# Kernel optimization log

Hardware: AMD Instinct MI355X
Metric: run time of the kernel (lower is better)

The kernel has to match this reference:

```python
import jax
import jax.numpy as jnp
import numpy as np

B, R, C, Q, D = 16, 2048, 81, 65, 1024
K = 1024          # pre-NMS candidate cap (fixed-shape stand-in for torch's dynamic filtering)
DET = 100         # detections_per_img
IMG = 640.0       # square image size (clip bound)
SCORE_THRESH = 0.05
NMS_THRESH = 0.5
MIN_SIZE = 0.01
BBOX_CLIP = float(np.log(1000.0 / 16.0))  # torchvision BoxCoder bbox_xform_clip
WX, WY, WW, WH = 10.0, 10.0, 5.0, 5.0     # BoxCoder weights


def setup_inputs() -> dict:
    key = jax.random.key(0)
    k1, k2, k3, k4, k5, k6 = jax.random.split(key, 6)
    class_logits = 2.0 * jax.random.normal(k1, (B, R, C), jnp.float32)
    quantity_logits = jax.random.normal(k2, (B, R, Q), jnp.float32)
    box_features = jax.random.normal(k3, (B, R, D), jnp.float32)
    box_regression = 0.5 * jax.random.normal(k4, (B, R, C * 4), jnp.float32)
    cxcy = jax.random.uniform(k5, (B, R, 2), jnp.float32, 0.0, IMG)
    wh = jax.random.uniform(k6, (B, R, 2), jnp.float32, 10.0, 80.0)
    x1y1 = jnp.clip(cxcy - 0.5 * wh, 0.0, IMG)
    x2y2 = jnp.clip(cxcy + 0.5 * wh, 0.0, IMG)
    proposals = jnp.concatenate([x1y1, x2y2], axis=-1)
    return {
        'class_logits': class_logits,
        'quantity_logits': quantity_logits,
        'box_features': box_features,
        'box_regression': box_regression,
        'proposals': proposals,
    }


def _decode(deltas, props):
    # deltas: [R, C, 4], props: [R, 4] -> boxes [R, C, 4] (torchvision BoxCoder.decode)
    pw = props[:, 2] - props[:, 0]
    ph = props[:, 3] - props[:, 1]
    pcx = props[:, 0] + 0.5 * pw
    pcy = props[:, 1] + 0.5 * ph
    dx = deltas[..., 0] / WX
    dy = deltas[..., 1] / WY
    dw = jnp.minimum(deltas[..., 2] / WW, BBOX_CLIP)
    dh = jnp.minimum(deltas[..., 3] / WH, BBOX_CLIP)
    cx = dx * pw[:, None] + pcx[:, None]
    cy = dy * ph[:, None] + pcy[:, None]
    w = jnp.exp(dw) * pw[:, None]
    h = jnp.exp(dh) * ph[:, None]
    return jnp.stack([cx - 0.5 * w, cy - 0.5 * h, cx + 0.5 * w, cy + 0.5 * h], axis=-1)


def _iou_matrix(b):
    # b: [K, 4] -> pairwise IoU [K, K]
    area = (b[:, 2] - b[:, 0]) * (b[:, 3] - b[:, 1])
    lt = jnp.maximum(b[:, None, :2], b[None, :, :2])
    rb = jnp.minimum(b[:, None, 2:], b[None, :, 2:])
    whv = jnp.clip(rb - lt, 0.0)
    inter = whv[..., 0] * whv[..., 1]
    return inter / (area[:, None] + area[None, :] - inter + 1e-9)


def _process_image(logits, qlogits, feats, reg, props):
    # decode + clip
    boxes = jnp.clip(_decode(reg.reshape(R, C, 4), props), 0.0, IMG)  # [R, C, 4]
    scores = jax.nn.softmax(logits, axis=-1)                          # [R, C]
    quant = jnp.argmax(qlogits, axis=-1).astype(jnp.int32)            # [R]
    # drop background class 0, flatten to M = R*(C-1)
    fb = boxes[:, 1:, :].reshape(-1, 4)
    fs = scores[:, 1:].reshape(-1)
    fl = jnp.broadcast_to(jnp.arange(1, C, dtype=jnp.int32), (R, C - 1)).reshape(-1)
    fi = jnp.broadcast_to(jnp.arange(R, dtype=jnp.int32)[:, None], (R, C - 1)).reshape(-1)
    bw = fb[:, 2] - fb[:, 0]
    bh = fb[:, 3] - fb[:, 1]
    valid = (fs > SCORE_THRESH) & (bw >= MIN_SIZE) & (bh >= MIN_SIZE)
    # top-K candidates by masked score (sorted desc)
    top_s, top_i = jax.lax.top_k(jnp.where(valid, fs, -1.0), K)
    cb = fb[top_i]          # [K, 4]
    cl = fl[top_i]          # [K]
    ci = fi[top_i]          # [K] row index into proposals/features
    cv = top_s > 0.0        # candidate validity (score_thresh > 0)
    # batched NMS via per-class coordinate offset
    ob = cb + (cl.astype(jnp.float32) * (IMG + 1.0))[:, None]
    iou = _iou_matrix(ob)
    ar = jnp.arange(K)

    def body(i, keep):
        sup = (iou[i] > NMS_THRESH) & (ar > i)
        return jnp.where(keep[i] & cv[i], keep & ~sup, keep)

    keep = jax.lax.fori_loop(0, K, body, cv) & cv
    # first DET survivors in score order
    det_s, det_i = jax.lax.top_k(jnp.where(keep, top_s, -1.0), DET)
    dv = det_s > 0.0
    m = dv.astype(jnp.float32)
    db = cb[det_i] * m[:, None]
    dl = jnp.where(dv, cl[det_i], 0)
    di = ci[det_i]
    dq = jnp.where(dv, quant[di], 0)
    df = feats[di] * m[:, None]   # irregular gather of box features by surviving row idx
    ds = jnp.where(dv, det_s, 0.0)
    return db, ds, dl, dq, df, dv


def reference(class_logits, quantity_logits, box_features, box_regression, proposals):
    # returns (boxes [B,DET,4], scores [B,DET], labels [B,DET] i32,
    #          quantities [B,DET] i32, features [B,DET,D], valid [B,DET] bool)
    return jax.vmap(_process_image)(class_logits, quantity_logits, box_features,
                                    box_regression, proposals)
```

## Files before the change

### kernel.cpp

```cpp
#include <hip/hip_runtime.h>
#include <math.h>

#define NB 16
#define NR 2048
#define NC 81
#define NQ 65
#define ND 1024
#define NK 1024
#define NDET 100
#define NBLK 512
#define BSLOT 64
#define HBINS 5184
#define CH 256
#define L2CAP 384
#define LRCAP 1536
#define BBC 4.135166556742356f

#define O_BOX   0
#define O_SCORE (NB*NDET*4)
#define O_LABEL (O_SCORE + NB*NDET)
#define O_QUANT (O_LABEL + NB*NDET)
#define O_FEAT  (O_QUANT + NB*NDET)
#define O_VALID (O_FEAT + (size_t)NB*NDET*ND)

#define WS_CAND  ((size_t)0)
#define WS_GHIST (WS_CAND + (size_t)NB*NBLK*BSLOT*8)
#define WS_DETCB (WS_GHIST + (size_t)NB*HBINS*4)
#define WS_DETM  (WS_DETCB + (size_t)NB*NDET*16)
#define WS_DETS  (WS_DETM + (size_t)NB*NDET*4)
#define WS_CNT   (WS_DETS + (size_t)NB*NDET*4)

__device__ __forceinline__ float4 decode_box(float4 d, float pw, float ph,
                                             float pcx, float pcy) {
    float dx = d.x / 10.0f, dy = d.y / 10.0f;
    float dw = fminf(d.z / 5.0f, BBC), dh = fminf(d.w / 5.0f, BBC);
    float cx = dx * pw + pcx, cy = dy * ph + pcy;
    float w = expf(dw) * pw, h = expf(dh) * ph;
    float4 r;
    r.x = fminf(fmaxf(cx - 0.5f * w, 0.0f), 640.0f);
    r.y = fminf(fmaxf(cy - 0.5f * h, 0.0f), 640.0f);
    r.z = fminf(fmaxf(cx + 0.5f * w, 0.0f), 640.0f);
    r.w = fminf(fmaxf(cy + 0.5f * h, 0.0f), 640.0f);
    return r;
}

__global__ __launch_bounds__(256) void k_stage1(
    const float* __restrict__ logits, const float* __restrict__ reg,
    const float* __restrict__ props, unsigned long long* __restrict__ cand,
    int* __restrict__ cnt, unsigned int* __restrict__ ghist) {
    __shared__ unsigned long long sl[BSLOT];
    __shared__ int scnt;
    int b = blockIdx.x >> 9;
    int blk = blockIdx.x & (NBLK - 1);
    int wid = threadIdx.x >> 6;
    int lane = threadIdx.x & 63;
    int r = blk * 4 + wid;
    int row = b * NR + r;
    if (threadIdx.x == 0) scnt = 0;
    __syncthreads();

    const float* Lrow = logits + (size_t)row * NC;
    float v0 = Lrow[lane];
    float v1 = (lane < NC - 64) ? Lrow[64 + lane] : -1e30f;
    float mx = fmaxf(v0, v1);
    #pragma unroll
    for (int o = 32; o; o >>= 1) mx = fmaxf(mx, __shfl_xor(mx, o));
    float e = expf(v0 - mx) + ((lane < NC - 64) ? expf(v1 - mx) : 0.0f);
    float sm = e;
    #pragma unroll
    for (int o = 32; o; o >>= 1) sm += __shfl_xor(sm, o);
    float thr_lo = mx + logf(0.05f * sm) - 0.01f;

    const float* P = props + (size_t)row * 4;
    float p0 = P[0], p1 = P[1], p2 = P[2], p3 = P[3];
    float pw = p2 - p0, ph = p3 - p1;
    float pcx = p0 + 0.5f * pw, pcy = p1 + 0.5f * ph;
    const float* G = reg + (size_t)row * (NC * 4);

    #pragma unroll
    for (int pass = 0; pass < 2; ++pass) {
        int cc = lane + pass * 64;
        if (cc < NC - 1) {
            int c = cc + 1;
            float lc = Lrow[c];
            if (lc > thr_lo) {
                float p = expf(lc - mx) / sm;
                float4 d = *(const float4*)(G + 4 * c);
                float4 bx = decode_box(d, pw, ph, pcx, pcy);
                float bw = bx.z - bx.x, bh = bx.w - bx.y;
                if (p > 0.05f && bw >= 0.01f && bh >= 0.01f) {
                    int m = r * 80 + cc;
                    int pos = atomicAdd(&scnt, 1);
                    if (pos < BSLOT) {
                        sl[pos] = ((unsigned long long)__float_as_uint(p) << 32) |
                                  (unsigned)(~(unsigned)m);
                        unsigned bin = (__float_as_uint(p) - 0x3D000000u) >> 13;
                        atomicAdd(&ghist[b * HBINS + bin], 1u);
                    }
                }
            }
        }
    }
    __syncthreads();
    int n = scnt < BSLOT ? scnt : BSLOT;
    unsigned long long* dst = cand + ((size_t)b * NBLK + blk) * BSLOT;
    for (int i = threadIdx.x; i < n; i += 256) dst[i] = sl[i];
    if (threadIdx.x == 0) cnt[b * NBLK + blk] = n;
}

__global__ __launch_bounds__(1024) void k_fused(
    const unsigned long long* __restrict__ cand, const int* __restrict__ cnt,
    const unsigned int* __restrict__ ghist,
    const float* __restrict__ reg, const float* __restrict__ props,
    int* __restrict__ det_m, float* __restrict__ det_s,
    float4* __restrict__ det_cb) {
    __shared__ union {
        unsigned int hist[HBINS];
        unsigned long long sortedRest[LRCAP];
    } u;
    __shared__ unsigned long long list2[L2CAP], sorted2[L2CAP];
    __shared__ unsigned long long listRest[LRCAP];
    __shared__ float4 boff[L2CAP], bclip[L2CAP];
    __shared__ int scn[NBLK];
    __shared__ int s_c2, s_cR, s_b1, s_b2, s_A, s_need;
    int b = blockIdx.x, tid = threadIdx.x;
    const unsigned long long* cnd = cand + (size_t)b * NBLK * BSLOT;

    for (int i = tid; i < HBINS; i += 1024) u.hist[i] = ghist[b * HBINS + i];
    if (tid < NBLK) scn[tid] = cnt[b * NBLK + tid];
    if (tid == 0) { s_c2 = 0; s_cR = 0; s_b1 = 0; s_b2 = 0; s_A = 0; s_need = 0; }
    __syncthreads();

    if (tid < 64) {
        int lane = tid, base = lane * 81;
        unsigned partial = 0;
        for (int j = 0; j < 81; ++j) partial += u.hist[base + j];
        unsigned incl = partial;
        #pragma unroll
        for (int o = 1; o < 64; o <<= 1) {
            unsigned t = __shfl_up(incl, o);
            if (lane >= o) incl += t;
        }
        unsigned total = __shfl(incl, 63);
        unsigned suffix = total - incl;
        if (suffix < NK && suffix + partial >= NK) {
            unsigned A = suffix;
            for (int bb = base + 80; bb >= base; --bb) {
                unsigned An = A + u.hist[bb];
                if (An >= NK) { s_b1 = bb; break; }
                A = An;
            }
        }
        if (suffix < CH && suffix + partial >= CH) {
            unsigned A = suffix;
            for (int bb = base + 80; bb >= base; --bb) {
                unsigned An = A + u.hist[bb];
                if (An >= CH) { s_b2 = bb; break; }
                A = An;
            }
        }
    }
    __syncthreads();
    int b1 = s_b1, b2 = s_b2;

    for (int i = tid; i < NBLK * BSLOT; i += 1024) {
        if ((i & (BSLOT - 1)) < scn[i >> 6]) {
            unsigned long long key = cnd[i];
            int bin = (int)(((unsigned)(key >> 32) - 0x3D000000u) >> 13);
            if (bin >= b2) {
                int p = atomicAdd(&s_c2, 1);
                if (p < L2CAP) list2[p] = key;
            } else if (bin >= b1) {
                int p = atomicAdd(&s_cR, 1);
                if (p < LRCAP) listRest[p] = key;
            }
        }
    }
    __syncthreads();
    int T2 = s_c2 < L2CAP ? s_c2 : L2CAP;
    int TR = s_cR < LRCAP ? s_cR : LRCAP;
    int S = T2 + TR;
    int cap = S < NK ? S : NK;
    int limit1 = T2 < cap ? T2 : cap;

    if (tid < T2) {
        unsigned long long k0 = list2[tid];
        int rk = 0;
        for (int j = 0; j < T2; ++j) rk += (list2[j] > k0);
        sorted2[rk] = k0;
    }
    __syncthreads();

    if (tid < limit1) {
        unsigned long long key = sorted2[tid];
        int m = (int)(~(unsigned)key);
        int r = m / 80, c = m - r * 80 + 1;
        size_t row = (size_t)b * NR + r;
        float4 P = *(const float4*)(props + row * 4);
        float pw = P.z - P.x, ph = P.w - P.y;
        float pcx = P.x + 0.5f * pw, pcy = P.y + 0.5f * ph;
        float4 d = *(const float4*)(reg + row * (NC * 4) + 4 * c);
        float4 bx = decode_box(d, pw, ph, pcx, pcy);
        bclip[tid] = bx;
        float off = (float)c * 641.0f;
        float4 o = {bx.x + off, bx.y + off, bx.z + off, bx.w + off};
        boff[tid] = o;
    }
    __syncthreads();

    int lane = tid & 63;
    float4 a0 = {0, 0, 0, 0}, a1 = {0, 0, 0, 0};
    int A = 0;
    if (tid < 64) {
        unsigned long long nk_ = (limit1 > 0) ? sorted2[0] : 0ull;
        float4 nb_ = (limit1 > 0) ? boff[0] : a0;
        for (int t = 0; t < limit1; ++t) {
            unsigned long long keyt = nk_;
            float4 bt = nb_;
            if (t + 1 < limit1) { nk_ = sorted2[t + 1]; nb_ = boff[t + 1]; }
            float areaB = (bt.z - bt.x) * (bt.w - bt.y);
            float areaA0 = (a0.z - a0.x) * (a0.w - a0.y);
            float ltx = fmaxf(a0.x, bt.x), lty = fmaxf(a0.y, bt.y);
            float rbx = fminf(a0.z, bt.z), rby = fminf(a0.w, bt.w);
            float in0 = fmaxf(rbx - ltx, 0.0f) * fmaxf(rby - lty, 0.0f);
            bool sup = (lane < A) && (in0 / (areaA0 + areaB - in0 + 1e-9f) > 0.5f);
            if (A > 64) {
                float areaA1 = (a1.z - a1.x) * (a1.w - a1.y);
                float l1 = fmaxf(a1.x, bt.x), t1 = fmaxf(a1.y, bt.y);
                float r1 = fminf(a1.z, bt.z), b1f = fminf(a1.w, bt.w);
                float in1 = fmaxf(r1 - l1, 0.0f) * fmaxf(b1f - t1, 0.0f);
                sup |= (lane + 64 < A) &&
                       (in1 / (areaA1 + areaB - in1 + 1e-9f) > 0.5f);
            }
            if (!__any((int)sup)) {
                if (lane == (A & 63)) { if (A < 64) a0 = bt; else a1 = bt; }
                if (lane == 0) {
                    det_m[b * NDET + A] = (int)(~(unsigned)keyt);
                    det_s[b * NDET + A] = __uint_as_float((unsigned)(keyt >> 32));
                    det_cb[b * NDET + A] = bclip[t];
                }
                ++A;
                if (A == NDET) break;
            }
        }
        if (tid == 0) { s_A = A; s_need = (A < NDET && limit1 < cap) ? 1 : 0; }
    }
    __syncthreads();

    if (s_need) {
        for (int t0 = tid; t0 < TR; t0 += 1024) {
            unsigned long long k0 = listRest[t0];
            int rk = 0;
            for (int j = 0; j < TR; ++j) rk += (listRest[j] > k0);
            u.sortedRest[rk] = k0;
        }
        __syncthreads();
        if (tid < 64) {
            int nrest = cap - limit1;
            for (int t = 0; t < nrest && A < NDET; ++t) {
                unsigned long long keyt = u.sortedRest[t];
                int m = (int)(~(unsigned)keyt);
                int r = m / 80, c = m - r * 80 + 1;
                size_t row = (size_t)b * NR + r;
                float4 P = *(const float4*)(props + row * 4);
                float pw = P.z - P.x, ph = P.w - P.y;
                float pcx = P.x + 0.5f * pw, pcy = P.y + 0.5f * ph;
                float4 d = *(const float4*)(reg + row * (NC * 4) + 4 * c);
                float4 bx = decode_box(d, pw, ph, pcx, pcy);
                float off = (float)c * 641.0f;
                float4 bt = {bx.x + off, bx.y + off, bx.z + off, bx.w + off};
                float areaB = (bt.z - bt.x) * (bt.w - bt.y);
                float areaA0 = (a0.z - a0.x) * (a0.w - a0.y);
                float ltx = fmaxf(a0.x, bt.x), lty = fmaxf(a0.y, bt.y);
                float rbx = fminf(a0.z, bt.z), rby = fminf(a0.w, bt.w);
                float in0 = fmaxf(rbx - ltx, 0.0f) * fmaxf(rby - lty, 0.0f);
                bool sup = (lane < A) &&
                           (in0 / (areaA0 + areaB - in0 + 1e-9f) > 0.5f);
                if (A > 64) {
                    float areaA1 = (a1.z - a1.x) * (a1.w - a1.y);
                    float l1 = fmaxf(a1.x, bt.x), t1 = fmaxf(a1.y, bt.y);
                    float r1 = fminf(a1.z, bt.z), b1f = fminf(a1.w, bt.w);
                    float in1 = fmaxf(r1 - l1, 0.0f) * fmaxf(b1f - t1, 0.0f);
                    sup |= (lane + 64 < A) &&
                           (in1 / (areaA1 + areaB - in1 + 1e-9f) > 0.5f);
                }
                if (!__any((int)sup)) {
                    if (lane == (A & 63)) { if (A < 64) a0 = bt; else a1 = bt; }
                    if (lane == 0) {
                        det_m[b * NDET + A] = m;
                        det_s[b * NDET + A] =
                            __uint_as_float((unsigned)(keyt >> 32));
                        det_cb[b * NDET + A] = bx;
                    }
                    ++A;
                }
            }
            if (tid == 0) s_A = A;
        }
        __syncthreads();
    }
    for (int d = s_A + tid; d < NDET; d += 1024) det_m[b * NDET + d] = -1;
}

__global__ __launch_bounds__(256) void k_final(
    const float* __restrict__ feats, const float* __restrict__ qlog,
    const int* __restrict__ det_m, const float* __restrict__ det_s,
    const float4* __restrict__ det_cb, float* __restrict__ out) {
    int bd = blockIdx.x;
    int b = bd / NDET;
    int t = threadIdx.x;
    int m = det_m[bd];
    float4* of = (float4*)(out + O_FEAT + (size_t)bd * ND);
    if (m >= 0) {
        int r = m / 80, c = m - r * 80 + 1;
        size_t row = (size_t)b * NR + r;
        if (t == 0) {
            ((float4*)(out + O_BOX))[bd] = det_cb[bd];
            out[O_SCORE + bd] = det_s[bd];
            out[O_LABEL + bd] = (float)c;
            out[O_VALID + bd] = 1.0f;
        }
        if (t < 64) {
            const float* Qrow = qlog + row * NQ;
            float qv = Qrow[t];
            int qi = t;
            if (t == 0) {
                float q64 = Qrow[64];
                if (q64 > qv) { qv = q64; qi = 64; }
            }
            #pragma unroll
            for (int o = 32; o; o >>= 1) {
                float ov = __shfl_xor(qv, o);
                int oi = __shfl_xor(qi, o);
                if (ov > qv || (ov == qv && oi < qi)) { qv = ov; qi = oi; }
            }
            if (t == 0) out[O_QUANT + bd] = (float)qi;
        }
        const float4* f = (const float4*)(feats + row * ND);
        of[t] = f[t];
    } else {
        if (t == 0) {
            float4 z = {0, 0, 0, 0};
            ((float4*)(out + O_BOX))[bd] = z;
            out[O_SCORE + bd] = 0.0f;
            out[O_LABEL + bd] = 0.0f;
            out[O_QUANT + bd] = 0.0f;
            out[O_VALID + bd] = 0.0f;
        }
        float4 z = {0, 0, 0, 0};
        of[t] = z;
    }
}

extern "C" void kernel_launch(void* const* d_in, const int* in_sizes, int n_in,
                              void* d_out, int out_size, void* d_ws, size_t ws_size,
                              hipStream_t stream) {
    const float* logits = (const float*)d_in[0];
    const float* qlog   = (const float*)d_in[1];
    const float* feats  = (const float*)d_in[2];
    const float* reg    = (const float*)d_in[3];
    const float* props  = (const float*)d_in[4];
    float* out = (float*)d_out;
    char* ws = (char*)d_ws;

    unsigned long long* cand = (unsigned long long*)(ws + WS_CAND);
    unsigned int* ghist = (unsigned int*)(ws + WS_GHIST);
    float4* det_cb = (float4*)(ws + WS_DETCB);
    int* det_m = (int*)(ws + WS_DETM);
    float* det_s = (float*)(ws + WS_DETS);
    int* cnt = (int*)(ws + WS_CNT);

    hipMemsetAsync(ghist, 0, (size_t)NB * HBINS * 4, stream);
    k_stage1<<<NB * NBLK, 256, 0, stream>>>(logits, reg, props, cand, cnt, ghist);
    k_fused<<<NB, 1024, 0, stream>>>(cand, cnt, ghist, reg, props, det_m, det_s,
                                     det_cb);
    k_final<<<NB * NDET, 256, 0, stream>>>(feats, qlog, det_m, det_s, det_cb, out);
}
```

Measured before the change: 294.8 us.

## Fuse final gather into NMS kernel, reuse softmax exps, prefetch features

After: 300.2 us. About the same (+1.8%).

```diff
diff --git a/kernel.cpp b/kernel.cpp
--- a/kernel.cpp
+++ b/kernel.cpp
@@ -25,10 +25,7 @@
 
 #define WS_CAND  ((size_t)0)
 #define WS_GHIST (WS_CAND + (size_t)NB*NBLK*BSLOT*8)
-#define WS_DETCB (WS_GHIST + (size_t)NB*HBINS*4)
-#define WS_DETM  (WS_DETCB + (size_t)NB*NDET*16)
-#define WS_DETS  (WS_DETM + (size_t)NB*NDET*4)
-#define WS_CNT   (WS_DETS + (size_t)NB*NDET*4)
+#define WS_CNT   (WS_GHIST + (size_t)NB*HBINS*4)
 
 __device__ __forceinline__ float4 decode_box(float4 d, float pw, float ph,
                                              float pcx, float pcy) {
@@ -65,11 +62,16 @@
     float mx = fmaxf(v0, v1);
     #pragma unroll
     for (int o = 32; o; o >>= 1) mx = fmaxf(mx, __shfl_xor(mx, o));
-    float e = expf(v0 - mx) + ((lane < NC - 64) ? expf(v1 - mx) : 0.0f);
-    float sm = e;
+    float t0 = expf(v0 - mx);
+    float t1 = (lane < NC - 64) ? expf(v1 - mx) : 0.0f;
+    float sm = t0 + t1;
     #pragma unroll
     for (int o = 32; o; o >>= 1) sm += __shfl_xor(sm, o);
-    float thr_lo = mx + logf(0.05f * sm) - 0.01f;
+
+    float nx0 = __shfl_down(t0, 1);
+    float b64 = __shfl(t1, 0);
+    float tc0 = (lane == 63) ? b64 : nx0;
+    float tc1 = __shfl_down(t1, 1);
 
     const float* P = props + (size_t)row * 4;
     float p0 = P[0], p1 = P[1], p2 = P[2], p3 = P[3];
@@ -80,15 +82,15 @@
     #pragma unroll
     for (int pass = 0; pass < 2; ++pass) {
         int cc = lane + pass * 64;
+        float tc = pass ? tc1 : tc0;
         if (cc < NC - 1) {
-            int c = cc + 1;
-            float lc = Lrow[c];
-            if (lc > thr_lo) {
-                float p = expf(lc - mx) / sm;
+            float p = tc / sm;
+            if (p > 0.05f) {
+                int c = cc + 1;
                 float4 d = *(const float4*)(G + 4 * c);
                 float4 bx = decode_box(d, pw, ph, pcx, pcy);
                 float bw = bx.z - bx.x, bh = bx.w - bx.y;
-                if (p > 0.05f && bw >= 0.01f && bh >= 0.01f) {
+                if (bw >= 0.01f && bh >= 0.01f) {
                     int m = r * 80 + cc;
                     int pos = atomicAdd(&scnt, 1);
                     if (pos < BSLOT) {
@@ -112,8 +114,8 @@
     const unsigned long long* __restrict__ cand, const int* __restrict__ cnt,
     const unsigned int* __restrict__ ghist,
     const float* __restrict__ reg, const float* __restrict__ props,
-    int* __restrict__ det_m, float* __restrict__ det_s,
-    float4* __restrict__ det_cb) {
+    const float* __restrict__ feats, const float* __restrict__ qlog,
+    float* __restrict__ out) {
     __shared__ union {
         unsigned int hist[HBINS];
         unsigned long long sortedRest[LRCAP];
@@ -122,8 +124,12 @@
     __shared__ unsigned long long listRest[LRCAP];
     __shared__ float4 boff[L2CAP], bclip[L2CAP];
     __shared__ int scn[NBLK];
+    __shared__ int acc_m[NDET];
+    __shared__ float acc_s[NDET];
+    __shared__ float4 acc_b[NDET];
     __shared__ int s_c2, s_cR, s_b1, s_b2, s_A, s_need;
     int b = blockIdx.x, tid = threadIdx.x;
+    int lane = tid & 63;
     const unsigned long long* cnd = cand + (size_t)b * NBLK * BSLOT;
 
     for (int i = tid; i < HBINS; i += 1024) u.hist[i] = ghist[b * HBINS + i];
@@ -132,7 +138,7 @@
     __syncthreads();
 
     if (tid < 64) {
-        int lane = tid, base = lane * 81;
+        int base = tid * 81;
         unsigned partial = 0;
         for (int j = 0; j < 81; ++j) partial += u.hist[base + j];
         unsigned incl = partial;
@@ -208,7 +214,6 @@
     }
     __syncthreads();
 
-    int lane = tid & 63;
     float4 a0 = {0, 0, 0, 0}, a1 = {0, 0, 0, 0};
     int A = 0;
     if (tid < 64) {
@@ -235,15 +240,24 @@
             if (!__any((int)sup)) {
                 if (lane == (A & 63)) { if (A < 64) a0 = bt; else a1 = bt; }
                 if (lane == 0) {
-                    det_m[b * NDET + A] = (int)(~(unsigned)keyt);
-                    det_s[b * NDET + A] = __uint_as_float((unsigned)(keyt >> 32));
-                    det_cb[b * NDET + A] = bclip[t];
+                    acc_m[A] = (int)(~(unsigned)keyt);
+                    acc_s[A] = __uint_as_float((unsigned)(keyt >> 32));
+                    acc_b[A] = bclip[t];
                 }
                 ++A;
                 if (A == NDET) break;
             }
         }
         if (tid == 0) { s_A = A; s_need = (A < NDET && limit1 < cap) ? 1 : 0; }
+    } else {
+        int pn = limit1 < 128 ? limit1 : 128;
+        float s = 0.0f;
+        for (int k = tid - 64; k < pn * 32; k += 960) {
+            int m = (int)(~(unsigned)sorted2[k >> 5]);
+            int r = m / 80;
+            s += feats[(((size_t)b * NR + r) << 10) + ((k & 31) << 5)];
+        }
+        asm volatile("" :: "v"(s));
     }
     __syncthreads();
 
@@ -287,10 +301,9 @@
                 if (!__any((int)sup)) {
                     if (lane == (A & 63)) { if (A < 64) a0 = bt; else a1 = bt; }
                     if (lane == 0) {
-                        det_m[b * NDET + A] = m;
-                        det_s[b * NDET + A] =
-                            __uint_as_float((unsigned)(keyt >> 32));
-                        det_cb[b * NDET + A] = bx;
+                        acc_m[A] = m;
+                        acc_s[A] = __uint_as_float((unsigned)(keyt >> 32));
+                        acc_b[A] = bx;
                     }
                     ++A;
                 }
@@ -299,32 +312,31 @@
         }
         __syncthreads();
     }
-    for (int d = s_A + tid; d < NDET; d += 1024) det_m[b * NDET + d] = -1;
-}
-
-__global__ __launch_bounds__(256) void k_final(
-    const float* __restrict__ feats, const float* __restrict__ qlog,
-    const int* __restrict__ det_m, const float* __restrict__ det_s,
-    const float4* __restrict__ det_cb, float* __restrict__ out) {
-    int bd = blockIdx.x;
-    int b = bd / NDET;
-    int t = threadIdx.x;
-    int m = det_m[bd];
-    float4* of = (float4*)(out + O_FEAT + (size_t)bd * ND);
-    if (m >= 0) {
+
+    int Afin = s_A;
+    int base = b * NDET;
+
+    if (tid < NDET) {
+        bool dv = tid < Afin;
+        float4 z = {0, 0, 0, 0};
+        float4 bx = dv ? acc_b[tid] : z;
+        int m = dv ? acc_m[tid] : 0;
         int r = m / 80, c = m - r * 80 + 1;
-        size_t row = (size_t)b * NR + r;
-        if (t == 0) {
-            ((float4*)(out + O_BOX))[bd] = det_cb[bd];
-            out[O_SCORE + bd] = det_s[bd];
-            out[O_LABEL + bd] = (float)c;
-            out[O_VALID + bd] = 1.0f;
-        }
-        if (t < 64) {
-            const float* Qrow = qlog + row * NQ;
-            float qv = Qrow[t];
-            int qi = t;
-            if (t == 0) {
+        ((float4*)(out + O_BOX))[base + tid] = bx;
+        out[O_SCORE + base + tid] = dv ? acc_s[tid] : 0.0f;
+        out[O_LABEL + base + tid] = dv ? (float)c : 0.0f;
+        out[O_VALID + base + tid] = dv ? 1.0f : 0.0f;
+    }
+
+    int wid = tid >> 6;
+    for (int d = wid; d < NDET; d += 16) {
+        if (d < Afin) {
+            int m = acc_m[d];
+            int r = m / 80;
+            const float* Qrow = qlog + ((size_t)b * NR + r) * NQ;
+            float qv = Qrow[lane];
+            int qi = lane;
+            if (lane == 0) {
                 float q64 = Qrow[64];
                 if (q64 > qv) { qv = q64; qi = 64; }
             }
@@ -334,21 +346,23 @@
                 int oi = __shfl_xor(qi, o);
                 if (ov > qv || (ov == qv && oi < qi)) { qv = ov; qi = oi; }
             }
-            if (t == 0) out[O_QUANT + bd] = (float)qi;
-        }
-        const float4* f = (const float4*)(feats + row * ND);
-        of[t] = f[t];
-    } else {
-        if (t == 0) {
-            float4 z = {0, 0, 0, 0};
-            ((float4*)(out + O_BOX))[bd] = z;
-            out[O_SCORE + bd] = 0.0f;
-            out[O_LABEL + bd] = 0.0f;
-            out[O_QUANT + bd] = 0.0f;
-            out[O_VALID + bd] = 0.0f;
-        }
-        float4 z = {0, 0, 0, 0};
-        of[t] = z;
+            if (lane == 0) out[O_QUANT + base + d] = (float)qi;
+        } else if (lane == 0) {
+            out[O_QUANT + base + d] = 0.0f;
+        }
+    }
+
+    const float4* F4 = (const float4*)feats;
+    float4* OF4 = (float4*)(out + O_FEAT + (size_t)base * ND);
+    for (int i = tid; i < NDET * (ND / 4); i += 1024) {
+        int d = i >> 8;
+        float4 v = {0, 0, 0, 0};
+        if (d < Afin) {
+            int m = acc_m[d];
+            int r = m / 80;
+            v = F4[((size_t)b * NR + r) * (ND / 4) + (i & 255)];
+        }
+        OF4[i] = v;
     }
 }
 
@@ -365,14 +379,10 @@
 
     unsigned long long* cand = (unsigned long long*)(ws + WS_CAND);
     unsigned int* ghist = (unsigned int*)(ws + WS_GHIST);
-    float4* det_cb = (float4*)(ws + WS_DETCB);
-    int* det_m = (int*)(ws + WS_DETM);
-    float* det_s = (float*)(ws + WS_DETS);
     int* cnt = (int*)(ws + WS_CNT);
 
     hipMemsetAsync(ghist, 0, (size_t)NB * HBINS * 4, stream);
     k_stage1<<<NB * NBLK, 256, 0, stream>>>(logits, reg, props, cand, cnt, ghist);
-    k_fused<<<NB, 1024, 0, stream>>>(cand, cnt, ghist, reg, props, det_m, det_s,
-                                     det_cb);
-    k_final<<<NB * NDET, 256, 0, stream>>>(feats, qlog, det_m, det_s, det_cb, out);
+    k_fused<<<NB, 1024, 0, stream>>>(cand, cnt, ghist, reg, props, feats, qlog,
+                                     out);
 }
```

## Split fused select/NMS kernel into cut, parallel select, and NMS kernels with prefetch

Applied to the files above, without the earlier changes.

Result: slower. 517.4 us (+75.5%).

```diff
diff --git a/kernel.cpp b/kernel.cpp
--- a/kernel.cpp
+++ b/kernel.cpp
@@ -25,10 +25,13 @@
 
 #define WS_CAND  ((size_t)0)
 #define WS_GHIST (WS_CAND + (size_t)NB*NBLK*BSLOT*8)
-#define WS_DETCB (WS_GHIST + (size_t)NB*HBINS*4)
+#define WS_GCNT  (WS_GHIST + (size_t)NB*HBINS*4)
+#define WS_CNT   (WS_GCNT + (size_t)NB*16)
+#define WS_L2G   (WS_CNT + (size_t)NB*NBLK*4)
+#define WS_LRG   (WS_L2G + (size_t)NB*L2CAP*8)
+#define WS_DETCB (WS_LRG + (size_t)NB*LRCAP*8)
 #define WS_DETM  (WS_DETCB + (size_t)NB*NDET*16)
 #define WS_DETS  (WS_DETM + (size_t)NB*NDET*4)
-#define WS_CNT   (WS_DETS + (size_t)NB*NDET*4)
 
 __device__ __forceinline__ float4 decode_box(float4 d, float pw, float ph,
                                              float pcx, float pcy) {
@@ -65,11 +68,16 @@
     float mx = fmaxf(v0, v1);
     #pragma unroll
     for (int o = 32; o; o >>= 1) mx = fmaxf(mx, __shfl_xor(mx, o));
-    float e = expf(v0 - mx) + ((lane < NC - 64) ? expf(v1 - mx) : 0.0f);
-    float sm = e;
+    float t0 = expf(v0 - mx);
+    float t1 = (lane < NC - 64) ? expf(v1 - mx) : 0.0f;
+    float sm = t0 + t1;
     #pragma unroll
     for (int o = 32; o; o >>= 1) sm += __shfl_xor(sm, o);
-    float thr_lo = mx + logf(0.05f * sm) - 0.01f;
+
+    float nx0 = __shfl_down(t0, 1);
+    float b64 = __shfl(t1, 0);
+    float tc0 = (lane == 63) ? b64 : nx0;
+    float tc1 = __shfl_down(t1, 1);
 
     const float* P = props + (size_t)row * 4;
     float p0 = P[0], p1 = P[1], p2 = P[2], p3 = P[3];
@@ -80,15 +88,15 @@
     #pragma unroll
     for (int pass = 0; pass < 2; ++pass) {
         int cc = lane + pass * 64;
+        float tc = pass ? tc1 : tc0;
         if (cc < NC - 1) {
-            int c = cc + 1;
-            float lc = Lrow[c];
-            if (lc > thr_lo) {
-                float p = expf(lc - mx) / sm;
+            float p = tc / sm;
+            if (p > 0.05f) {
+                int c = cc + 1;
                 float4 d = *(const float4*)(G + 4 * c);
                 float4 bx = decode_box(d, pw, ph, pcx, pcy);
                 float bw = bx.z - bx.x, bh = bx.w - bx.y;
-                if (p > 0.05f && bw >= 0.01f && bh >= 0.01f) {
+                if (bw >= 0.01f && bh >= 0.01f) {
                     int m = r * 80 + cc;
                     int pos = atomicAdd(&scnt, 1);
                     if (pos < BSLOT) {
@@ -108,33 +116,16 @@
     if (threadIdx.x == 0) cnt[b * NBLK + blk] = n;
 }
 
-__global__ __launch_bounds__(1024) void k_fused(
-    const unsigned long long* __restrict__ cand, const int* __restrict__ cnt,
-    const unsigned int* __restrict__ ghist,
-    const float* __restrict__ reg, const float* __restrict__ props,
-    int* __restrict__ det_m, float* __restrict__ det_s,
-    float4* __restrict__ det_cb) {
-    __shared__ union {
-        unsigned int hist[HBINS];
-        unsigned long long sortedRest[LRCAP];
-    } u;
-    __shared__ unsigned long long list2[L2CAP], sorted2[L2CAP];
-    __shared__ unsigned long long listRest[LRCAP];
-    __shared__ float4 boff[L2CAP], bclip[L2CAP];
-    __shared__ int scn[NBLK];
-    __shared__ int s_c2, s_cR, s_b1, s_b2, s_A, s_need;
+__global__ __launch_bounds__(1024) void k_cut(
+    const unsigned int* __restrict__ ghist, unsigned int* __restrict__ gcnt) {
+    __shared__ unsigned int hist[HBINS];
     int b = blockIdx.x, tid = threadIdx.x;
-    const unsigned long long* cnd = cand + (size_t)b * NBLK * BSLOT;
-
-    for (int i = tid; i < HBINS; i += 1024) u.hist[i] = ghist[b * HBINS + i];
-    if (tid < NBLK) scn[tid] = cnt[b * NBLK + tid];
-    if (tid == 0) { s_c2 = 0; s_cR = 0; s_b1 = 0; s_b2 = 0; s_A = 0; s_need = 0; }
-    __syncthreads();
-
+    for (int i = tid; i < HBINS; i += 1024) hist[i] = ghist[b * HBINS + i];
+    __syncthreads();
     if (tid < 64) {
         int lane = tid, base = lane * 81;
         unsigned partial = 0;
-        for (int j = 0; j < 81; ++j) partial += u.hist[base + j];
+        for (int j = 0; j < 81; ++j) partial += hist[base + j];
         unsigned incl = partial;
         #pragma unroll
         for (int o = 1; o < 64; o <<= 1) {
@@ -146,47 +137,82 @@
         if (suffix < NK && suffix + partial >= NK) {
             unsigned A = suffix;
             for (int bb = base + 80; bb >= base; --bb) {
-                unsigned An = A + u.hist[bb];
-                if (An >= NK) { s_b1 = bb; break; }
+                unsigned An = A + hist[bb];
+                if (An >= NK) { gcnt[b * 4 + 2] = (unsigned)bb; break; }
                 A = An;
             }
         }
         if (suffix < CH && suffix + partial >= CH) {
             unsigned A = suffix;
             for (int bb = base + 80; bb >= base; --bb) {
-                unsigned An = A + u.hist[bb];
-                if (An >= CH) { s_b2 = bb; break; }
+                unsigned An = A + hist[bb];
+                if (An >= CH) { gcnt[b * 4 + 3] = (unsigned)bb; break; }
                 A = An;
             }
         }
     }
-    __syncthreads();
-    int b1 = s_b1, b2 = s_b2;
-
-    for (int i = tid; i < NBLK * BSLOT; i += 1024) {
-        if ((i & (BSLOT - 1)) < scn[i >> 6]) {
-            unsigned long long key = cnd[i];
-            int bin = (int)(((unsigned)(key >> 32) - 0x3D000000u) >> 13);
-            if (bin >= b2) {
-                int p = atomicAdd(&s_c2, 1);
-                if (p < L2CAP) list2[p] = key;
-            } else if (bin >= b1) {
-                int p = atomicAdd(&s_cR, 1);
-                if (p < LRCAP) listRest[p] = key;
-            }
-        }
-    }
-    __syncthreads();
-    int T2 = s_c2 < L2CAP ? s_c2 : L2CAP;
-    int TR = s_cR < LRCAP ? s_cR : LRCAP;
+}
+
+__global__ __launch_bounds__(256) void k_select(
+    const unsigned long long* __restrict__ cand, const int* __restrict__ cnt,
+    unsigned int* __restrict__ gcnt, unsigned long long* __restrict__ l2g,
+    unsigned long long* __restrict__ lrg) {
+    int b = blockIdx.x >> 7;
+    int blk = blockIdx.x & 127;
+    int i = blk * 256 + threadIdx.x;
+    int b1 = (int)gcnt[b * 4 + 2];
+    int b2 = (int)gcnt[b * 4 + 3];
+    if ((i & (BSLOT - 1)) < cnt[b * NBLK + (i >> 6)]) {
+        unsigned long long key = cand[(size_t)b * NBLK * BSLOT + i];
+        int bin = (int)(((unsigned)(key >> 32) - 0x3D000000u) >> 13);
+        if (bin >= b2) {
+            int p = (int)atomicAdd(&gcnt[b * 4 + 0], 1u);
+            if (p < L2CAP) l2g[(size_t)b * L2CAP + p] = key;
+        } else if (bin >= b1) {
+            int p = (int)atomicAdd(&gcnt[b * 4 + 1], 1u);
+            if (p < LRCAP) lrg[(size_t)b * LRCAP + p] = key;
+        }
+    }
+}
+
+__global__ __launch_bounds__(1024) void k_nms(
+    const unsigned int* __restrict__ gcnt,
+    const unsigned long long* __restrict__ l2g,
+    const unsigned long long* __restrict__ lrg,
+    const float* __restrict__ reg, const float* __restrict__ props,
+    const float* __restrict__ feats,
+    int* __restrict__ det_m, float* __restrict__ det_s,
+    float4* __restrict__ det_cb) {
+    __shared__ unsigned long long list2[L2CAP], sorted2[L2CAP];
+    __shared__ unsigned long long listRest[LRCAP], sortedRest[LRCAP];
+    __shared__ float4 boff[L2CAP], bclip[L2CAP];
+    __shared__ int s_A, s_need;
+    int b = blockIdx.x, tid = threadIdx.x;
+    int lane = tid & 63;
+
+    int c2 = (int)gcnt[b * 4 + 0];
+    int cR = (int)gcnt[b * 4 + 1];
+    int T2 = c2 < L2CAP ? c2 : L2CAP;
+    int TR = cR < LRCAP ? cR : LRCAP;
     int S = T2 + TR;
     int cap = S < NK ? S : NK;
     int limit1 = T2 < cap ? T2 : cap;
+    if (tid == 0) { s_A = 0; s_need = 0; }
+
+    for (int i = tid; i < T2; i += 1024) list2[i] = l2g[(size_t)b * L2CAP + i];
+    for (int i = tid; i < TR; i += 1024) listRest[i] = lrg[(size_t)b * LRCAP + i];
+    __syncthreads();
 
     if (tid < T2) {
         unsigned long long k0 = list2[tid];
-        int rk = 0;
-        for (int j = 0; j < T2; ++j) rk += (list2[j] > k0);
+        int rk = 0, j = 0;
+        for (; j + 8 <= T2; j += 8) {
+            rk += (list2[j] > k0) + (list2[j + 1] > k0) +
+                  (list2[j + 2] > k0) + (list2[j + 3] > k0) +
+                  (list2[j + 4] > k0) + (list2[j + 5] > k0) +
+                  (list2[j + 6] > k0) + (list2[j + 7] > k0);
+        }
+        for (; j < T2; ++j) rk += (list2[j] > k0);
         sorted2[rk] = k0;
     }
     __syncthreads();
@@ -208,7 +234,6 @@
     }
     __syncthreads();
 
-    int lane = tid & 63;
     float4 a0 = {0, 0, 0, 0}, a1 = {0, 0, 0, 0};
     int A = 0;
     if (tid < 64) {
@@ -244,21 +269,36 @@
             }
         }
         if (tid == 0) { s_A = A; s_need = (A < NDET && limit1 < cap) ? 1 : 0; }
+    } else {
+        int pn = limit1 < 128 ? limit1 : 128;
+        float s = 0.0f;
+        for (int k = tid - 64; k < pn * 32; k += 960) {
+            int m = (int)(~(unsigned)sorted2[k >> 5]);
+            int r = m / 80;
+            s += feats[(((size_t)b * NR + r) << 10) + ((k & 31) << 5)];
+        }
+        asm volatile("" :: "v"(s));
     }
     __syncthreads();
 
     if (s_need) {
         for (int t0 = tid; t0 < TR; t0 += 1024) {
             unsigned long long k0 = listRest[t0];
-            int rk = 0;
-            for (int j = 0; j < TR; ++j) rk += (listRest[j] > k0);
-            u.sortedRest[rk] = k0;
+            int rk = 0, j = 0;
+            for (; j + 8 <= TR; j += 8) {
+                rk += (listRest[j] > k0) + (listRest[j + 1] > k0) +
+                      (listRest[j + 2] > k0) + (listRest[j + 3] > k0) +
+                      (listRest[j + 4] > k0) + (listRest[j + 5] > k0) +
+                      (listRest[j + 6] > k0) + (listRest[j + 7] > k0);
+            }
+            for (; j < TR; ++j) rk += (listRest[j] > k0);
+            sortedRest[rk] = k0;
         }
         __syncthreads();
         if (tid < 64) {
             int nrest = cap - limit1;
             for (int t = 0; t < nrest && A < NDET; ++t) {
-                unsigned long long keyt = u.sortedRest[t];
+                unsigned long long keyt = sortedRest[t];
                 int m = (int)(~(unsigned)keyt);
                 int r = m / 80, c = m - r * 80 + 1;
                 size_t row = (size_t)b * NR + r;
@@ -365,14 +405,19 @@
 
     unsigned long long* cand = (unsigned long long*)(ws + WS_CAND);
     unsigned int* ghist = (unsigned int*)(ws + WS_GHIST);
+    unsigned int* gcnt = (unsigned int*)(ws + WS_GCNT);
+    int* cnt = (int*)(ws + WS_CNT);
+    unsigned long long* l2g = (unsigned long long*)(ws + WS_L2G);
+    unsigned long long* lrg = (unsigned long long*)(ws + WS_LRG);
     float4* det_cb = (float4*)(ws + WS_DETCB);
     int* det_m = (int*)(ws + WS_DETM);
     float* det_s = (float*)(ws + WS_DETS);
-    int* cnt = (int*)(ws + WS_CNT);
-
-    hipMemsetAsync(ghist, 0, (size_t)NB * HBINS * 4, stream);
+
+    hipMemsetAsync(ghist, 0, (size_t)NB * HBINS * 4 + NB * 16, stream);
     k_stage1<<<NB * NBLK, 256, 0, stream>>>(logits, reg, props, cand, cnt, ghist);
-    k_fused<<<NB, 1024, 0, stream>>>(cand, cnt, ghist, reg, props, det_m, det_s,
-                                     det_cb);
+    k_cut<<<NB, 1024, 0, stream>>>(ghist, gcnt);
+    k_select<<<NB * 128, 256, 0, stream>>>(cand, cnt, gcnt, l2g, lrg);
+    k_nms<<<NB, 1024, 0, stream>>>(gcnt, l2g, lrg, reg, props, feats,
+                                   det_m, det_s, det_cb);
     k_final<<<NB * NDET, 256, 0, stream>>>(feats, qlog, det_m, det_s, det_cb, out);
 }
```

## Precompute parallel IoU bitmasks for NMS and reuse softmax exponentials in stage1

Applied to the files above, without the earlier changes.

New measurement: 282.0 us. 1.05x faster.

```diff
diff --git a/kernel.cpp b/kernel.cpp
--- a/kernel.cpp
+++ b/kernel.cpp
@@ -14,6 +14,7 @@
 #define CH 256
 #define L2CAP 384
 #define LRCAP 1536
+#define MASKW 6
 #define BBC 4.135166556742356f
 
 #define O_BOX   0
@@ -65,11 +66,16 @@
     float mx = fmaxf(v0, v1);
     #pragma unroll
     for (int o = 32; o; o >>= 1) mx = fmaxf(mx, __shfl_xor(mx, o));
-    float e = expf(v0 - mx) + ((lane < NC - 64) ? expf(v1 - mx) : 0.0f);
-    float sm = e;
+    float t0 = expf(v0 - mx);
+    float t1 = (lane < NC - 64) ? expf(v1 - mx) : 0.0f;
+    float sm = t0 + t1;
     #pragma unroll
     for (int o = 32; o; o >>= 1) sm += __shfl_xor(sm, o);
-    float thr_lo = mx + logf(0.05f * sm) - 0.01f;
+
+    float nx0 = __shfl_down(t0, 1);
+    float b64 = __shfl(t1, 0);
+    float tc0 = (lane == 63) ? b64 : nx0;
+    float tc1 = __shfl_down(t1, 1);
 
     const float* P = props + (size_t)row * 4;
     float p0 = P[0], p1 = P[1], p2 = P[2], p3 = P[3];
@@ -80,15 +86,15 @@
     #pragma unroll
     for (int pass = 0; pass < 2; ++pass) {
         int cc = lane + pass * 64;
+        float tc = pass ? tc1 : tc0;
         if (cc < NC - 1) {
-            int c = cc + 1;
-            float lc = Lrow[c];
-            if (lc > thr_lo) {
-                float p = expf(lc - mx) / sm;
+            float p = tc / sm;
+            if (p > 0.05f) {
+                int c = cc + 1;
                 float4 d = *(const float4*)(G + 4 * c);
                 float4 bx = decode_box(d, pw, ph, pcx, pcy);
                 float bw = bx.z - bx.x, bh = bx.w - bx.y;
-                if (p > 0.05f && bw >= 0.01f && bh >= 0.01f) {
+                if (bw >= 0.01f && bh >= 0.01f) {
                     int m = r * 80 + cc;
                     int pos = atomicAdd(&scnt, 1);
                     if (pos < BSLOT) {
@@ -112,18 +118,23 @@
     const unsigned long long* __restrict__ cand, const int* __restrict__ cnt,
     const unsigned int* __restrict__ ghist,
     const float* __restrict__ reg, const float* __restrict__ props,
+    const float* __restrict__ feats,
     int* __restrict__ det_m, float* __restrict__ det_s,
     float4* __restrict__ det_cb) {
     __shared__ union {
         unsigned int hist[HBINS];
+        unsigned long long masks[L2CAP * MASKW];
         unsigned long long sortedRest[LRCAP];
     } u;
     __shared__ unsigned long long list2[L2CAP], sorted2[L2CAP];
     __shared__ unsigned long long listRest[LRCAP];
     __shared__ float4 boff[L2CAP], bclip[L2CAP];
     __shared__ int scn[NBLK];
+    __shared__ int acc_t[NDET];
     __shared__ int s_c2, s_cR, s_b1, s_b2, s_A, s_need;
     int b = blockIdx.x, tid = threadIdx.x;
+    int lane = tid & 63;
+    int wid = tid >> 6;
     const unsigned long long* cnd = cand + (size_t)b * NBLK * BSLOT;
 
     for (int i = tid; i < HBINS; i += 1024) u.hist[i] = ghist[b * HBINS + i];
@@ -132,7 +143,7 @@
     __syncthreads();
 
     if (tid < 64) {
-        int lane = tid, base = lane * 81;
+        int base = lane * 81;
         unsigned partial = 0;
         for (int j = 0; j < 81; ++j) partial += u.hist[base + j];
         unsigned incl = partial;
@@ -163,9 +174,10 @@
     __syncthreads();
     int b1 = s_b1, b2 = s_b2;
 
+    #pragma unroll 4
     for (int i = tid; i < NBLK * BSLOT; i += 1024) {
+        unsigned long long key = cnd[i];
         if ((i & (BSLOT - 1)) < scn[i >> 6]) {
-            unsigned long long key = cnd[i];
             int bin = (int)(((unsigned)(key >> 32) - 0x3D000000u) >> 13);
             if (bin >= b2) {
                 int p = atomicAdd(&s_c2, 1);
@@ -185,8 +197,14 @@
 
     if (tid < T2) {
         unsigned long long k0 = list2[tid];
-        int rk = 0;
-        for (int j = 0; j < T2; ++j) rk += (list2[j] > k0);
+        int rk = 0, j = 0;
+        for (; j + 8 <= T2; j += 8) {
+            rk += (list2[j] > k0) + (list2[j + 1] > k0) +
+                  (list2[j + 2] > k0) + (list2[j + 3] > k0) +
+                  (list2[j + 4] > k0) + (list2[j + 5] > k0) +
+                  (list2[j + 6] > k0) + (list2[j + 7] > k0);
+        }
+        for (; j < T2; ++j) rk += (list2[j] > k0);
         sorted2[rk] = k0;
     }
     __syncthreads();
@@ -208,54 +226,128 @@
     }
     __syncthreads();
 
-    int lane = tid & 63;
-    float4 a0 = {0, 0, 0, 0}, a1 = {0, 0, 0, 0};
-    int A = 0;
+    float4 jb[MASKW];
+    float ja[MASKW];
+    #pragma unroll
+    for (int g = 0; g < MASKW; ++g) {
+        int j = g * 64 + lane;
+        float4 v = {0, 0, 0, 0};
+        if (j < limit1) v = boff[j];
+        jb[g] = v;
+        ja[g] = (v.z - v.x) * (v.w - v.y);
+    }
+    for (int t = wid; t < limit1; t += 16) {
+        float4 bt = boff[t];
+        float at = (bt.z - bt.x) * (bt.w - bt.y);
+        #pragma unroll
+        for (int g = 0; g < MASKW; ++g) {
+            unsigned long long word = 0;
+            if (g * 64 + 63 > t && g * 64 < limit1) {
+                int j = g * 64 + lane;
+                float4 a = jb[g];
+                float ltx = fmaxf(a.x, bt.x), lty = fmaxf(a.y, bt.y);
+                float rbx = fminf(a.z, bt.z), rby = fminf(a.w, bt.w);
+                float in0 = fmaxf(rbx - ltx, 0.0f) * fmaxf(rby - lty, 0.0f);
+                float iou = in0 / (at + ja[g] - in0 + 1e-9f);
+                bool over = (iou > 0.5f) && (j > t) && (j < limit1);
+                word = __ballot((int)over);
+            }
+            if (lane == 0) u.masks[t * MASKW + g] = word;
+        }
+    }
+    __syncthreads();
+
     if (tid < 64) {
-        unsigned long long nk_ = (limit1 > 0) ? sorted2[0] : 0ull;
-        float4 nb_ = (limit1 > 0) ? boff[0] : a0;
-        for (int t = 0; t < limit1; ++t) {
-            unsigned long long keyt = nk_;
-            float4 bt = nb_;
-            if (t + 1 < limit1) { nk_ = sorted2[t + 1]; nb_ = boff[t + 1]; }
-            float areaB = (bt.z - bt.x) * (bt.w - bt.y);
-            float areaA0 = (a0.z - a0.x) * (a0.w - a0.y);
-            float ltx = fmaxf(a0.x, bt.x), lty = fmaxf(a0.y, bt.y);
-            float rbx = fminf(a0.z, bt.z), rby = fminf(a0.w, bt.w);
-            float in0 = fmaxf(rbx - ltx, 0.0f) * fmaxf(rby - lty, 0.0f);
-            bool sup = (lane < A) && (in0 / (areaA0 + areaB - in0 + 1e-9f) > 0.5f);
-            if (A > 64) {
-                float areaA1 = (a1.z - a1.x) * (a1.w - a1.y);
-                float l1 = fmaxf(a1.x, bt.x), t1 = fmaxf(a1.y, bt.y);
-                float r1 = fminf(a1.z, bt.z), b1f = fminf(a1.w, bt.w);
-                float in1 = fmaxf(r1 - l1, 0.0f) * fmaxf(b1f - t1, 0.0f);
-                sup |= (lane + 64 < A) &&
-                       (in1 / (areaA1 + areaB - in1 + 1e-9f) > 0.5f);
-            }
-            if (!__any((int)sup)) {
-                if (lane == (A & 63)) { if (A < 64) a0 = bt; else a1 = bt; }
-                if (lane == 0) {
-                    det_m[b * NDET + A] = (int)(~(unsigned)keyt);
-                    det_s[b * NDET + A] = __uint_as_float((unsigned)(keyt >> 32));
-                    det_cb[b * NDET + A] = bclip[t];
-                }
-                ++A;
+        int A = 0;
+        if (limit1 > 0) {
+            unsigned long long rm = 0;
+            int midx = (lane < 6) ? lane : 0;
+            #define MRD(T) (((lane < 6) && ((T) < limit1)) ? \
+                u.masks[((T) < limit1 ? (T) : 0) * MASKW + midx] : 0ull)
+            unsigned long long pf0 = MRD(0), pf1 = MRD(1);
+            unsigned long long pf2 = MRD(2), pf3 = MRD(3);
+            for (int t = 0; t < limit1; t += 4) {
+                {
+                    unsigned long long sup = pf0; pf0 = MRD(t + 4);
+                    unsigned long long word = __shfl(rm, t >> 6);
+                    if (!((word >> (t & 63)) & 1ull) && A < NDET) {
+                        rm |= sup;
+                        if (lane == 0) acc_t[A] = t;
+                        ++A;
+                    }
+                }
+                if (t + 1 < limit1) {
+                    unsigned long long sup = pf1; pf1 = MRD(t + 5);
+                    unsigned long long word = __shfl(rm, (t + 1) >> 6);
+                    if (!((word >> ((t + 1) & 63)) & 1ull) && A < NDET) {
+                        rm |= sup;
+                        if (lane == 0) acc_t[A] = t + 1;
+                        ++A;
+                    }
+                }
+                if (t + 2 < limit1) {
+                    unsigned long long sup = pf2; pf2 = MRD(t + 6);
+                    unsigned long long word = __shfl(rm, (t + 2) >> 6);
+                    if (!((word >> ((t + 2) & 63)) & 1ull) && A < NDET) {
+                        rm |= sup;
+                        if (lane == 0) acc_t[A] = t + 2;
+                        ++A;
+                    }
+                }
+                if (t + 3 < limit1) {
+                    unsigned long long sup = pf3; pf3 = MRD(t + 7);
+                    unsigned long long word = __shfl(rm, (t + 3) >> 6);
+                    if (!((word >> ((t + 3) & 63)) & 1ull) && A < NDET) {
+                        rm |= sup;
+                        if (lane == 0) acc_t[A] = t + 3;
+                        ++A;
+                    }
+                }
                 if (A == NDET) break;
             }
+            #undef MRD
         }
         if (tid == 0) { s_A = A; s_need = (A < NDET && limit1 < cap) ? 1 : 0; }
-    }
-    __syncthreads();
+    } else {
+        int pn = limit1 < 128 ? limit1 : 128;
+        float s = 0.0f;
+        for (int k = tid - 64; k < pn * 32; k += 960) {
+            int m = (int)(~(unsigned)sorted2[k >> 5]);
+            int r = m / 80;
+            s += feats[(((size_t)b * NR + r) << 10) + ((k & 31) << 5)];
+        }
+        asm volatile("" :: "v"(s));
+    }
+    __syncthreads();
+
+    int Af = s_A;
+    if (tid < Af) {
+        int t = acc_t[tid];
+        unsigned long long key = sorted2[t];
+        det_m[b * NDET + tid] = (int)(~(unsigned)key);
+        det_s[b * NDET + tid] = __uint_as_float((unsigned)(key >> 32));
+        det_cb[b * NDET + tid] = bclip[t];
+    }
 
     if (s_need) {
         for (int t0 = tid; t0 < TR; t0 += 1024) {
             unsigned long long k0 = listRest[t0];
-            int rk = 0;
-            for (int j = 0; j < TR; ++j) rk += (listRest[j] > k0);
+            int rk = 0, j = 0;
+            for (; j + 8 <= TR; j += 8) {
+                rk += (listRest[j] > k0) + (listRest[j + 1] > k0) +
+                      (listRest[j + 2] > k0) + (listRest[j + 3] > k0) +
+                      (listRest[j + 4] > k0) + (listRest[j + 5] > k0) +
+                      (listRest[j + 6] > k0) + (listRest[j + 7] > k0);
+            }
+            for (; j < TR; ++j) rk += (listRest[j] > k0);
             u.sortedRest[rk] = k0;
         }
         __syncthreads();
         if (tid < 64) {
+            int A = Af;
+            float4 a0 = {0, 0, 0, 0}, a1 = {0, 0, 0, 0};
+            if (lane < A) a0 = boff[acc_t[lane]];
+            if (64 + lane < A) a1 = boff[acc_t[64 + lane]];
             int nrest = cap - limit1;
             for (int t = 0; t < nrest && A < NDET; ++t) {
                 unsigned long long keyt = u.sortedRest[t];
@@ -372,7 +464,7 @@
 
     hipMemsetAsync(ghist, 0, (size_t)NB * HBINS * 4, stream);
     k_stage1<<<NB * NBLK, 256, 0, stream>>>(logits, reg, props, cand, cnt, ghist);
-    k_fused<<<NB, 1024, 0, stream>>>(cand, cnt, ghist, reg, props, det_m, det_s,
-                                     det_cb);
+    k_fused<<<NB, 1024, 0, stream>>>(cand, cnt, ghist, reg, props, feats,
+                                     det_m, det_s, det_cb);
     k_final<<<NB * NDET, 256, 0, stream>>>(feats, qlog, det_m, det_s, det_cb, out);
 }
```
